# Optimization experiments

Hardware: AMD Instinct MI355X
Metric: run time of the kernel (lower is better)

## Reference

```python
import math
import jax, jax.numpy as jnp
import numpy as np

N0 = N1 = 100000
E = 200000
IN = OUT = 128
H = 8
DK = OUT // H
T = 2
R = 3


def setup_inputs() -> dict:
    key = jax.random.key(0)
    ks = jax.random.split(key, 24)
    s = 1.0 / math.sqrt(IN)
    inp = {
        'h0': jax.random.normal(ks[0], (N0, IN), jnp.float32),
        'h1': jax.random.normal(ks[1], (N1, IN), jnp.float32),
        'kw': jax.random.normal(ks[2], (T, IN, OUT), jnp.float32) * s,
        'kb': jax.random.normal(ks[3], (T, OUT), jnp.float32) * 0.01,
        'qw': jax.random.normal(ks[4], (T, IN, OUT), jnp.float32) * s,
        'qb': jax.random.normal(ks[5], (T, OUT), jnp.float32) * 0.01,
        'vw': jax.random.normal(ks[6], (T, IN, OUT), jnp.float32) * s,
        'vb': jax.random.normal(ks[7], (T, OUT), jnp.float32) * 0.01,
        'aw': jax.random.normal(ks[8], (T, OUT, OUT), jnp.float32) * (1.0 / math.sqrt(OUT)),
        'ab': jax.random.normal(ks[9], (T, OUT), jnp.float32) * 0.01,
        'rel_att': jax.random.normal(ks[10], (R, H, DK, DK), jnp.float32) * (1.0 / math.sqrt(DK)),
        'rel_msg': jax.random.normal(ks[11], (R, H, DK, DK), jnp.float32) * (1.0 / math.sqrt(DK)),
        'rel_pri': jnp.ones((R, H), jnp.float32),
        'skip': jnp.ones((T,), jnp.float32),
        'src0': jax.random.randint(ks[12], (E,), 0, N1, jnp.int32),  # author -> paper
        'dst0': jax.random.randint(ks[13], (E,), 0, N0, jnp.int32),
        'src1': jax.random.randint(ks[14], (E,), 0, N0, jnp.int32),  # paper -> author
        'dst1': jax.random.randint(ks[15], (E,), 0, N1, jnp.int32),
        'src2': jax.random.randint(ks[16], (E,), 0, N0, jnp.int32),  # paper -> paper
        'dst2': jax.random.randint(ks[17], (E,), 0, N0, jnp.int32),
    }
    return inp


def _edge_softmax(score, dst, n_dst):
    # segment softmax normalized by destination node (norm_by='dst')
    m = jax.ops.segment_max(score, dst, num_segments=n_dst)
    e = jnp.exp(score - m[dst])
    s = jax.ops.segment_sum(e, dst, num_segments=n_dst)
    return e / s[dst]


def reference(h0, h1, kw, kb, qw, qb, vw, vb, aw, ab, rel_att, rel_msg,
              rel_pri, skip, src0, dst0, src1, dst1, src2, dst2):
    n_heads, d_k = rel_att.shape[1], rel_att.shape[2]
    sqrt_dk = math.sqrt(d_k)
    hs = (h0, h1)
    Ns = (h0.shape[0], h1.shape[0])
    # per-type K/Q/V projections, reshaped to [N, H, d_k]
    k = [(hs[t] @ kw[t] + kb[t]).reshape(-1, n_heads, d_k) for t in range(2)]
    q = [(hs[t] @ qw[t] + qb[t]).reshape(-1, n_heads, d_k) for t in range(2)]
    v = [(hs[t] @ vw[t] + vb[t]).reshape(-1, n_heads, d_k) for t in range(2)]
    # (relation id, src node type, dst node type, src idx, dst idx)
    rels = ((0, 1, 0, src0, dst0), (1, 0, 1, src1, dst1), (2, 0, 0, src2, dst2))
    agg = {0: [], 1: []}
    for r, st, dt, s_idx, d_idx in rels:
        kk = jnp.einsum('nij,ijk->nik', k[st], rel_att[r])
        vv = jnp.einsum('nij,ijk->nik', v[st], rel_msg[r])
        score = (q[dt][d_idx] * kk[s_idx]).sum(-1) * rel_pri[r] / sqrt_dk  # [E,H]
        attn = _edge_softmax(score, d_idx, Ns[dt])
        msg = vv[s_idx] * attn[..., None]  # [E,H,d_k]
        agg[dt].append(jax.ops.segment_sum(msg, d_idx, num_segments=Ns[dt]))
    outs = []
    for t in range(2):
        tt = sum(agg[t]) / len(agg[t])  # cross_reducer='mean'
        tt = tt.reshape(Ns[t], n_heads * d_k)
        trans = tt @ aw[t] + ab[t]  # dropout in eval mode -> identity
        alpha = jax.nn.sigmoid(skip[t])
        outs.append(trans * alpha + hs[t] * (1.0 - alpha))
    return jnp.stack(outs)  # [2, N, out_dim] (N0 == N1)
```

## Files before the change

### kernel.cpp

```cpp
#include <hip/hip_runtime.h>
#include <stdint.h>

typedef __attribute__((ext_vector_type(8))) short s16x8;
typedef __attribute__((ext_vector_type(4))) float f32x4;

__device__ __forceinline__ ushort f2bf(float x) {
  union { float f; uint32_t u; } v; v.f = x;
  uint32_t r = v.u + 0x7FFFu + ((v.u >> 16) & 1u);
  return (ushort)(r >> 16);
}
__device__ __forceinline__ float bf2f(ushort u) {
  union { uint32_t u; float f; } v; v.u = ((uint32_t)u) << 16; return v.f;
}

__device__ __forceinline__ void barrier_lds_only() {
  asm volatile("s_waitcnt lgkmcnt(0)" ::: "memory");
  __builtin_amdgcn_s_barrier();
}

__global__ __launch_bounds__(256) void prep_weights(
    const float* __restrict__ kw, const float* __restrict__ kb,
    const float* __restrict__ qw, const float* __restrict__ qb,
    const float* __restrict__ vw, const float* __restrict__ vb,
    const float* __restrict__ aw, const float* __restrict__ ab,
    const float* __restrict__ rel_att, const float* __restrict__ rel_msg,
    ushort* __restrict__ WT, float* __restrict__ BIAS)
{
  int slot = blockIdx.x, tid = threadIdx.x;
  const float* W; const float* b; const float* rel = nullptr;
  switch (slot) {
    case 0: W = qw;         b = qb;       break;
    case 1: W = qw + 16384; b = qb + 128; break;
    case 2: W = kw + 16384; b = kb + 128; rel = rel_att + 0*2048; break;
    case 3: W = kw;         b = kb;       rel = rel_att + 1*2048; break;
    case 4: W = kw;         b = kb;       rel = rel_att + 2*2048; break;
    case 5: W = vw + 16384; b = vb + 128; rel = rel_msg + 0*2048; break;
    case 6: W = vw;         b = vb;       rel = rel_msg + 1*2048; break;
    case 7: W = vw;         b = vb;       rel = rel_msg + 2*2048; break;
    case 8: W = aw;         b = ab;       break;
    default: W = aw + 16384; b = ab + 128; break;
  }
  ushort* out = WT + slot * 16384;
  for (int e = tid; e < 16384; e += 256) {
    int c = e >> 7, k = e & 127;
    float val;
    if (!rel) {
      val = W[k*128 + c];
    } else {
      int h = c >> 4, cc = c & 15;
      float s = 0.f;
      #pragma unroll
      for (int j = 0; j < 16; j++) s += W[k*128 + h*16 + j] * rel[h*256 + j*16 + cc];
      val = s;
    }
    out[c*128 + k] = f2bf(val);
  }
  if (tid < 128) {
    int c = tid; float val;
    if (!rel) {
      val = b[c];
    } else {
      int h = c >> 4, cc = c & 15;
      float s = 0.f;
      #pragma unroll
      for (int j = 0; j < 16; j++) s += b[h*16 + j] * rel[h*256 + j*16 + cc];
      val = s;
    }
    BIAS[slot*128 + c] = val;
  }
}

__global__ __launch_bounds__(256) void proj_fused(
    const float* __restrict__ h0, const float* __restrict__ h1,
    const ushort* __restrict__ WT, const float* __restrict__ BIAS,
    ushort* __restrict__ P, int N)
{
  __shared__ ushort ALDS0[64 * 132];
  __shared__ ushort ALDS1[64 * 132];

  int src_t = blockIdx.y;
  const float* A = src_t ? h1 : h0;
  int nslots = src_t ? 3 : 5;
  unsigned smap = src_t ? 0x521u : 0x76430u;

  int tid = threadIdx.x;
  int lane = tid & 63;
  int wave = tid >> 6;
  int lr = lane & 15, lh = lane >> 4;
  int colbase = (wave & 1) * 64;
  int rowhalf = wave >> 1;

  int base = blockIdx.x * 64;
  if (base >= N) return;

  s16x8 af[2][4];
  #pragma unroll
  for (int rg = 0; rg < 2; rg++) {
    int arow = base + rowhalf*32 + rg*16 + lr;
    if (arow >= N) arow = N - 1;
    #pragma unroll
    for (int ks = 0; ks < 4; ks++) {
      const float* ap = A + (size_t)arow*128 + ks*32 + lh*8;
      f32x4 x0 = *(const f32x4*)ap;
      f32x4 x1 = *(const f32x4*)(ap + 4);
      s16x8 v;
      #pragma unroll
      for (int j = 0; j < 4; j++) { v[j] = (short)f2bf(x0[j]); v[4+j] = (short)f2bf(x1[j]); }
      af[rg][ks] = v;
    }
  }

  auto compute_slot = [&](int g, ushort* L) {
    const ushort* Bt = WT + g * 16384;
    const float* bias = BIAS + g * 128;
    #pragma unroll
    for (int ct = 0; ct < 4; ct++) {
      int col = colbase + ct*16 + lr;
      s16x8 bfr[4];
      #pragma unroll
      for (int ks = 0; ks < 4; ks++)
        bfr[ks] = *(const s16x8*)(Bt + col*128 + ks*32 + lh*8);
      float bb = bias[col];
      #pragma unroll
      for (int rg = 0; rg < 2; rg++) {
        f32x4 acc = { bb, bb, bb, bb };
        #pragma unroll
        for (int ks = 0; ks < 4; ks++)
          acc = __builtin_amdgcn_mfma_f32_16x16x32_bf16(af[rg][ks], bfr[ks], acc, 0, 0, 0);
        int rl0 = rowhalf*32 + rg*16 + lh*4;
        #pragma unroll
        for (int i = 0; i < 4; i++)
          L[(rl0 + i) * 132 + col] = f2bf(acc[i]);
      }
    }
  };

  auto copyout = [&](int g, const ushort* L) {
    ushort* C = P + (size_t)g * N * 128;
    #pragma unroll
    for (int j = 0; j < 4; j++) {
      int idx = j * 256 + tid;
      int row = idx >> 4, ch = idx & 15;
      int gr = base + row;
      if (gr < N)
        __builtin_nontemporal_store(
            *(const s16x8*)(L + row * 132 + ch * 8),
            (s16x8*)(C + (size_t)gr * 128 + ch * 8));
    }
  };

  int prev = smap & 15;
  compute_slot(prev, ALDS0);
  barrier_lds_only();
  for (int si = 1; si < nslots; si++) {
    int g = (smap >> (si * 4)) & 15;
    ushort* cur = (si & 1) ? ALDS1 : ALDS0;
    const ushort* pv = (si & 1) ? ALDS0 : ALDS1;
    copyout(prev, pv);
    compute_slot(g, cur);
    barrier_lds_only();
    prev = g;
  }
  copyout(prev, (nslots & 1) ? ALDS0 : ALDS1);
}

__global__ void count_edges(const int* __restrict__ d0, const int* __restrict__ d1,
                            const int* __restrict__ d2, int* __restrict__ counts,
                            int E, int N)
{
  int idx = blockIdx.x * 256 + threadIdx.x;
  if (idx >= 3 * E) return;
  int r = idx / E, e = idx - r * E;
  const int* D = (r == 0) ? d0 : (r == 1) ? d1 : d2;
  atomicAdd(counts + r * N + D[e], 1);
}

#define SCAN_CHUNK 2048
#define MAXC 1024

__global__ __launch_bounds__(256) void scan_partial(
    const int* __restrict__ counts, int* __restrict__ offsets,
    int* __restrict__ bsum, int N)
{
  int r = blockIdx.y, c = blockIdx.x, tid = threadIdx.x;
  const int* cnt = counts + (size_t)r * N;
  int* o = offsets + (size_t)r * (N + 1);
  int idx0 = c * SCAN_CHUNK + tid * 8;
  int p[8]; int run = 0;
  #pragma unroll
  for (int j = 0; j < 8; j++) {
    int v = (idx0 + j < N) ? cnt[idx0 + j] : 0;
    run += v; p[j] = run;
  }
  int lane = tid & 63, wid = tid >> 6;
  int x = run;
  #pragma unroll
  for (int off = 1; off < 64; off <<= 1) {
    int t = __shfl_up(x, off, 64);
    if (lane >= off) x += t;
  }
  __shared__ int wsum[4];
  if (lane == 63) wsum[wid] = x;
  __syncthreads();
  int woff = 0;
  for (int wph = 0; wph < wid; wph++) woff += wsum[wph];
  int texcl = woff + x - run;
  #pragma unroll
  for (int j = 0; j < 8; j++)
    if (idx0 + j < N) o[idx0 + j + 1] = texcl + p[j];
  if (tid == 255) bsum[r * MAXC + c] = woff + x;
}

__global__ void scan_bsums(int* __restrict__ bsum, int nchunks)
{
  int r = blockIdx.x, lane = threadIdx.x;
  int carry = 0;
  for (int base = 0; base < nchunks; base += 64) {
    int i = base + lane;
    int v0 = (i < nchunks) ? bsum[r * MAXC + i] : 0;
    int x = v0;
    #pragma unroll
    for (int off = 1; off < 64; off <<= 1) {
      int t = __shfl_up(x, off, 64);
      if (lane >= off) x += t;
    }
    if (i < nchunks) bsum[r * MAXC + i] = carry + x - v0;
    carry += __shfl(x, 63, 64);
  }
}

__global__ __launch_bounds__(256) void scan_add(
    int* __restrict__ offsets, const int* __restrict__ bsum, int N)
{
  int r = blockIdx.y, c = blockIdx.x, tid = threadIdx.x;
  int* o = offsets + (size_t)r * (N + 1);
  if (c == 0 && tid == 0) o[0] = 0;
  int add = bsum[r * MAXC + c];
  if (add == 0) return;
  int idx0 = c * SCAN_CHUNK + tid * 8;
  #pragma unroll
  for (int j = 0; j < 8; j++) {
    int i = idx0 + j;
    if (i < N) o[i + 1] += add;
  }
}

__global__ void scatter_edges(const int* __restrict__ d0, const int* __restrict__ d1,
                              const int* __restrict__ d2,
                              const int* __restrict__ offsets, int* __restrict__ cursor,
                              int* __restrict__ elist, int E, int N)
{
  int idx = blockIdx.x * 256 + threadIdx.x;
  if (idx >= 3 * E) return;
  int r = idx / E, e = idx - r * E;
  const int* D = (r == 0) ? d0 : (r == 1) ? d1 : d2;
  int dst = D[e];
  int pos = offsets[r * (N + 1) + dst] + atomicAdd(cursor + r * N + dst, 1);
  elist[r * E + pos] = e;
}

__global__ __launch_bounds__(256) void agg_final(
    const int* __restrict__ elistA, const int* __restrict__ offsA,
    const int* __restrict__ SA,
    const ushort* __restrict__ KKA, const ushort* __restrict__ VVA,
    const int* __restrict__ elistB, const int* __restrict__ offsB,
    const int* __restrict__ SB,
    const ushort* __restrict__ KKB, const ushort* __restrict__ VVB,
    int nrel, int rA, int rB,
    const ushort* __restrict__ Q, const float* __restrict__ rel_pri,
    const ushort* __restrict__ WT, const float* __restrict__ BIAS,
    const float* __restrict__ H, const float* __restrict__ skip, int t,
    float* __restrict__ outT, int N)
{
  __shared__ ushort ALDS[32 * 132];

  int tid = threadIdx.x;
  int dstl = tid >> 3, h = tid & 7;
  int dst = blockIdx.x * 32 + dstl;
  bool valid = dst < N;

  float qf[16];
  {
    const ushort* qrow = Q + (size_t)(valid ? dst : 0) * 128 + h * 16;
    s16x8 qa = *(const s16x8*)qrow;
    s16x8 qb_ = *(const s16x8*)(qrow + 8);
    #pragma unroll
    for (int j = 0; j < 8; j++) { qf[j] = bf2f((ushort)qa[j]); qf[8 + j] = bf2f((ushort)qb_[j]); }
  }

  float accT[16];
  #pragma unroll
  for (int j = 0; j < 16; j++) accT[j] = 0.f;

  {
    float pr = rel_pri[rA * 8 + h] * 0.25f;
    int b0 = valid ? offsA[dst] : 0, b1 = valid ? offsA[dst + 1] : 0;
    float sum = 0.f;
    float acc[16];
    #pragma unroll
    for (int j = 0; j < 16; j++) acc[j] = 0.f;
    for (int i = b0; i < b1; i++) {
      int e = elistA[i];
      int s = SA[e];
      const ushort* kr = KKA + (size_t)s * 128 + h * 16;
      s16x8 k0 = *(const s16x8*)kr;
      s16x8 k1 = *(const s16x8*)(kr + 8);
      float sc = 0.f;
      #pragma unroll
      for (int j = 0; j < 8; j++)
        sc += qf[j] * bf2f((ushort)k0[j]) + qf[8 + j] * bf2f((ushort)k1[j]);
      float w = __expf(sc * pr);
      const ushort* vr = VVA + (size_t)s * 128 + h * 16;
      s16x8 v0 = *(const s16x8*)vr;
      s16x8 v1 = *(const s16x8*)(vr + 8);
      #pragma unroll
      for (int j = 0; j < 8; j++) {
        acc[j]     += w * bf2f((ushort)v0[j]);
        acc[8 + j] += w * bf2f((ushort)v1[j]);
      }
      sum += w;
    }
    float inv = (b1 > b0) ? 1.0f / sum : 0.f;
    #pragma unroll
    for (int j = 0; j < 16; j++) accT[j] += acc[j] * inv;
  }
  if (nrel == 2) {
    float pr = rel_pri[rB * 8 + h] * 0.25f;
    int b0 = valid ? offsB[dst] : 0, b1 = valid ? offsB[dst + 1] : 0;
    float sum = 0.f;
    float acc[16];
    #pragma unroll
    for (int j = 0; j < 16; j++) acc[j] = 0.f;
    for (int i = b0; i < b1; i++) {
      int e = elistB[i];
      int s = SB[e];
      const ushort* kr = KKB + (size_t)s * 128 + h * 16;
      s16x8 k0 = *(const s16x8*)kr;
      s16x8 k1 = *(const s16x8*)(kr + 8);
      float sc = 0.f;
      #pragma unroll
      for (int j = 0; j < 8; j++)
        sc += qf[j] * bf2f((ushort)k0[j]) + qf[8 + j] * bf2f((ushort)k1[j]);
      float w = __expf(sc * pr);
      const ushort* vr = VVB + (size_t)s * 128 + h * 16;
      s16x8 v0 = *(const s16x8*)vr;
      s16x8 v1 = *(const s16x8*)(vr + 8);
      #pragma unroll
      for (int j = 0; j < 8; j++) {
        acc[j]     += w * bf2f((ushort)v0[j]);
        acc[8 + j] += w * bf2f((ushort)v1[j]);
      }
      sum += w;
    }
    float inv = (b1 > b0) ? 1.0f / sum : 0.f;
    #pragma unroll
    for (int j = 0; j < 16; j++) accT[j] += acc[j] * inv;
  }
  float sc = (nrel == 2) ? 0.5f : 1.0f;
  ushort* arow = ALDS + dstl * 132 + h * 16;
  #pragma unroll
  for (int j = 0; j < 16; j++) arow[j] = f2bf(accT[j] * sc);

  __syncthreads();

  int lane = tid & 63, wv = tid >> 6;
  int lr = lane & 15, lh = lane >> 4;
  int rowhalf = wv & 1, colhalf = wv >> 1;
  const ushort* Bt = WT + (8 + t) * 16384;
  const float* bias = BIAS + (8 + t) * 128;
  float alpha = 1.0f / (1.0f + __expf(-skip[t]));
  float beta = 1.0f - alpha;

  s16x8 af[4];
  int arow_l = rowhalf * 16 + lr;
  #pragma unroll
  for (int ks = 0; ks < 4; ks++)
    af[ks] = *(const s16x8*)(ALDS + arow_l * 132 + ks * 32 + lh * 8);

  #pragma unroll
  for (int ct = 0; ct < 4; ct++) {
    int col = colhalf * 64 + ct * 16 + lr;
    s16x8 bfr[4];
    #pragma unroll
    for (int ks = 0; ks < 4; ks++)
      bfr[ks] = *(const s16x8*)(Bt + col * 128 + ks * 32 + lh * 8);
    float bb = bias[col];
    f32x4 acc = { bb, bb, bb, bb };
    #pragma unroll
    for (int ks = 0; ks < 4; ks++)
      acc = __builtin_amdgcn_mfma_f32_16x16x32_bf16(af[ks], bfr[ks], acc, 0, 0, 0);
    int r0l = rowhalf * 16 + lh * 4;
    #pragma unroll
    for (int i = 0; i < 4; i++) {
      int g = blockIdx.x * 32 + r0l + i;
      if (g < N) {
        size_t off = (size_t)g * 128 + col;
        __builtin_nontemporal_store(acc[i] * alpha + H[off] * beta, &outT[off]);
      }
    }
  }
}

extern "C" void kernel_launch(void* const* d_in, const int* in_sizes, int n_in,
                              void* d_out, int out_size, void* d_ws, size_t ws_size,
                              hipStream_t stream)
{
  const float* h0      = (const float*)d_in[0];
  const float* h1      = (const float*)d_in[1];
  const float* kw      = (const float*)d_in[2];
  const float* kb      = (const float*)d_in[3];
  const float* qw      = (const float*)d_in[4];
  const float* qb      = (const float*)d_in[5];
  const float* vw      = (const float*)d_in[6];
  const float* vb      = (const float*)d_in[7];
  const float* aw      = (const float*)d_in[8];
  const float* ab      = (const float*)d_in[9];
  const float* rel_att = (const float*)d_in[10];
  const float* rel_msg = (const float*)d_in[11];
  const float* rel_pri = (const float*)d_in[12];
  const float* skip    = (const float*)d_in[13];
  const int* s0 = (const int*)d_in[14];
  const int* d0 = (const int*)d_in[15];
  const int* s1 = (const int*)d_in[16];
  const int* d1 = (const int*)d_in[17];
  const int* s2 = (const int*)d_in[18];
  const int* d2 = (const int*)d_in[19];

  int N = in_sizes[0] / 128;
  int E = in_sizes[14];

  char* w = (char*)d_ws;
  size_t o = 0;
  auto alloc = [&](size_t bytes) { size_t cur = o; o += (bytes + 255) / 256 * 256; return cur; };
  ushort* WT   = (ushort*)(w + alloc((size_t)10 * 16384 * 2));
  float*  BIAS = (float*) (w + alloc((size_t)10 * 128 * 4));
  ushort* P    = (ushort*)(w + alloc((size_t)8 * N * 128 * 2));
  int* counts  = (int*)   (w + alloc((size_t)3 * N * 4));
  int* cursor  = (int*)   (w + alloc((size_t)3 * N * 4));
  int* offs    = (int*)   (w + alloc((size_t)3 * (N + 1) * 4));
  int* elist   = (int*)   (w + alloc((size_t)3 * E * 4));
  int* bsum    = (int*)   (w + alloc((size_t)3 * MAXC * 4));
  (void)ws_size; (void)n_in; (void)out_size;

  hipMemsetAsync(counts, 0, (size_t)3 * N * 4, stream);
  hipMemsetAsync(cursor, 0, (size_t)3 * N * 4, stream);

  prep_weights<<<10, 256, 0, stream>>>(kw, kb, qw, qb, vw, vb, aw, ab,
                                       rel_att, rel_msg, WT, BIAS);

  proj_fused<<<dim3((N + 63) / 64, 2), 256, 0, stream>>>(h0, h1, WT, BIAS, P, N);

  int egrid = (3 * E + 255) / 256;
  count_edges<<<egrid, 256, 0, stream>>>(d0, d1, d2, counts, E, N);

  int nchunks = (N + SCAN_CHUNK - 1) / SCAN_CHUNK;
  scan_partial<<<dim3(nchunks, 3), 256, 0, stream>>>(counts, offs, bsum, N);
  scan_bsums<<<3, 64, 0, stream>>>(bsum, nchunks);
  scan_add<<<dim3(nchunks, 3), 256, 0, stream>>>(offs, bsum, N);

  scatter_edges<<<egrid, 256, 0, stream>>>(d0, d1, d2, offs, cursor, elist, E, N);

  int fgrid = (N + 31) / 32;
  agg_final<<<fgrid, 256, 0, stream>>>(
      elist + (size_t)0 * E, offs + (size_t)0 * (N + 1), s0,
      P + (size_t)2 * N * 128, P + (size_t)5 * N * 128,
      elist + (size_t)2 * E, offs + (size_t)2 * (N + 1), s2,
      P + (size_t)4 * N * 128, P + (size_t)7 * N * 128,
      2, 0, 2,
      P + (size_t)0 * N * 128, rel_pri,
      WT, BIAS, h0, skip, 0, (float*)d_out, N);
  agg_final<<<fgrid, 256, 0, stream>>>(
      elist + (size_t)1 * E, offs + (size_t)1 * (N + 1), s1,
      P + (size_t)3 * N * 128, P + (size_t)6 * N * 128,
      elist + (size_t)1 * E, offs + (size_t)1 * (N + 1), s1,
      P + (size_t)3 * N * 128, P + (size_t)6 * N * 128,
      1, 1, 1,
      P + (size_t)1 * N * 128, rel_pri,
      WT, BIAS, h1, skip, 1, (float*)d_out + (size_t)N * 128, N);
}
```

Baseline: 414.5 us.

## Fold relation matrices into query and output weights instead of per-source K/V

Moves the per-relation att matrix from the key side onto the query (q·W_att^T) and the per-relation msg matrix into the output projection (W_msg·aw), so only plain K and V per node type are projected and stored (4 slabs instead of 8). The per-relation query projections are computed inside the aggregation kernel with MFMA from H rows, and the final projection sums two relation-specific GEMMs. This halves the projection GEMM work and projected-feature traffic, at the cost of extra MFMA work and LDS buffers in the aggregation kernel.

```diff
diff --git a/kernel.cpp b/kernel.cpp
--- a/kernel.cpp
+++ b/kernel.cpp
@@ -27,44 +27,50 @@
     ushort* __restrict__ WT, float* __restrict__ BIAS)
 {
   int slot = blockIdx.x, tid = threadIdx.x;
-  const float* W; const float* b; const float* rel = nullptr;
+  const float* W; const float* b; const float* rel = nullptr; int mode;
   switch (slot) {
-    case 0: W = qw;         b = qb;       break;
-    case 1: W = qw + 16384; b = qb + 128; break;
-    case 2: W = kw + 16384; b = kb + 128; rel = rel_att + 0*2048; break;
-    case 3: W = kw;         b = kb;       rel = rel_att + 1*2048; break;
-    case 4: W = kw;         b = kb;       rel = rel_att + 2*2048; break;
-    case 5: W = vw + 16384; b = vb + 128; rel = rel_msg + 0*2048; break;
-    case 6: W = vw;         b = vb;       rel = rel_msg + 1*2048; break;
-    case 7: W = vw;         b = vb;       rel = rel_msg + 2*2048; break;
-    case 8: W = aw;         b = ab;       break;
-    default: W = aw + 16384; b = ab + 128; break;
+    case 0: W = kw;         b = kb;       mode = 0; break;
+    case 1: W = kw + 16384; b = kb + 128; mode = 0; break;
+    case 2: W = vw;         b = vb;       mode = 0; break;
+    case 3: W = vw + 16384; b = vb + 128; mode = 0; break;
+    case 4: W = qw;         b = qb;       rel = rel_att;        mode = 1; break;
+    case 5: W = qw + 16384; b = qb + 128; rel = rel_att + 2048; mode = 1; break;
+    case 6: W = qw;         b = qb;       rel = rel_att + 4096; mode = 1; break;
+    case 7: W = aw;         b = ab;       rel = rel_msg;        mode = 2; break;
+    case 8: W = aw + 16384; b = ab + 128; rel = rel_msg + 2048; mode = 2; break;
+    default: W = aw;        b = ab;       rel = rel_msg + 4096; mode = 2; break;
   }
   ushort* out = WT + slot * 16384;
   for (int e = tid; e < 16384; e += 256) {
     int c = e >> 7, k = e & 127;
     float val;
-    if (!rel) {
+    if (mode == 0) {
       val = W[k*128 + c];
-    } else {
+    } else if (mode == 1) {
       int h = c >> 4, cc = c & 15;
       float s = 0.f;
       #pragma unroll
-      for (int j = 0; j < 16; j++) s += W[k*128 + h*16 + j] * rel[h*256 + j*16 + cc];
+      for (int j = 0; j < 16; j++) s += W[k*128 + h*16 + j] * rel[h*256 + cc*16 + j];
+      val = s;
+    } else {
+      int hr = k >> 4, ir = k & 15;
+      float s = 0.f;
+      #pragma unroll
+      for (int j = 0; j < 16; j++) s += rel[hr*256 + ir*16 + j] * W[(hr*16 + j)*128 + c];
       val = s;
     }
     out[c*128 + k] = f2bf(val);
   }
   if (tid < 128) {
     int c = tid; float val;
-    if (!rel) {
-      val = b[c];
-    } else {
+    if (mode == 1) {
       int h = c >> 4, cc = c & 15;
       float s = 0.f;
       #pragma unroll
-      for (int j = 0; j < 16; j++) s += b[h*16 + j] * rel[h*256 + j*16 + cc];
+      for (int j = 0; j < 16; j++) s += b[h*16 + j] * rel[h*256 + cc*16 + j];
       val = s;
+    } else {
+      val = b[c];
     }
     BIAS[slot*128 + c] = val;
   }
@@ -80,8 +86,8 @@
 
   int src_t = blockIdx.y;
   const float* A = src_t ? h1 : h0;
-  int nslots = src_t ? 3 : 5;
-  unsigned smap = src_t ? 0x521u : 0x76430u;
+  unsigned smap = src_t ? 0x31u : 0x20u;
+  const int nslots = 2;
 
   int tid = threadIdx.x;
   int lane = tid & 63;
@@ -154,14 +160,12 @@
   barrier_lds_only();
   for (int si = 1; si < nslots; si++) {
     int g = (smap >> (si * 4)) & 15;
-    ushort* cur = (si & 1) ? ALDS1 : ALDS0;
-    const ushort* pv = (si & 1) ? ALDS0 : ALDS1;
-    copyout(prev, pv);
-    compute_slot(g, cur);
+    copyout(prev, ALDS0);
+    compute_slot(g, ALDS1);
     barrier_lds_only();
     prev = g;
   }
-  copyout(prev, (nslots & 1) ? ALDS0 : ALDS1);
+  copyout(prev, ALDS1);
 }
 
 __global__ void count_edges(const int* __restrict__ d0, const int* __restrict__ d1,
@@ -262,140 +266,222 @@
 __global__ __launch_bounds__(256) void agg_final(
     const int* __restrict__ elistA, const int* __restrict__ offsA,
     const int* __restrict__ SA,
-    const ushort* __restrict__ KKA, const ushort* __restrict__ VVA,
+    const ushort* __restrict__ KA, const ushort* __restrict__ VA,
     const int* __restrict__ elistB, const int* __restrict__ offsB,
     const int* __restrict__ SB,
-    const ushort* __restrict__ KKB, const ushort* __restrict__ VVB,
+    const ushort* __restrict__ KB, const ushort* __restrict__ VB,
     int nrel, int rA, int rB,
-    const ushort* __restrict__ Q, const float* __restrict__ rel_pri,
+    int qslotA, int qslotB, int fslotA, int fslotB,
     const ushort* __restrict__ WT, const float* __restrict__ BIAS,
-    const float* __restrict__ H, const float* __restrict__ skip, int t,
+    const float* __restrict__ H, const float* __restrict__ rel_pri,
+    const float* __restrict__ skip, int t,
     float* __restrict__ outT, int N)
 {
-  __shared__ ushort ALDS[32 * 132];
+  __shared__ ushort T0[32 * 132];
+  __shared__ ushort T1[32 * 132];
 
   int tid = threadIdx.x;
+  int lane = tid & 63, wv = tid >> 6;
+  int lr = lane & 15, lh = lane >> 4;
+  int rowhalf = wv & 1, colhalf = wv >> 1;
+  int base = blockIdx.x * 32;
+
+  s16x8 af[4];
+  {
+    int arow = base + rowhalf*16 + lr;
+    if (arow >= N) arow = N - 1;
+    #pragma unroll
+    for (int ks = 0; ks < 4; ks++) {
+      const float* ap = H + (size_t)arow*128 + ks*32 + lh*8;
+      f32x4 x0 = *(const f32x4*)ap;
+      f32x4 x1 = *(const f32x4*)(ap + 4);
+      s16x8 v;
+      #pragma unroll
+      for (int j = 0; j < 4; j++) { v[j] = (short)f2bf(x0[j]); v[4+j] = (short)f2bf(x1[j]); }
+      af[ks] = v;
+    }
+  }
+  {
+    const ushort* Bt = WT + qslotA * 16384;
+    const float* bq = BIAS + qslotA * 128;
+    #pragma unroll
+    for (int ct = 0; ct < 4; ct++) {
+      int col = colhalf*64 + ct*16 + lr;
+      s16x8 bfr[4];
+      #pragma unroll
+      for (int ks = 0; ks < 4; ks++)
+        bfr[ks] = *(const s16x8*)(Bt + col*128 + ks*32 + lh*8);
+      float bb = bq[col];
+      f32x4 acc = { bb, bb, bb, bb };
+      #pragma unroll
+      for (int ks = 0; ks < 4; ks++)
+        acc = __builtin_amdgcn_mfma_f32_16x16x32_bf16(af[ks], bfr[ks], acc, 0, 0, 0);
+      int r0l = rowhalf*16 + lh*4;
+      #pragma unroll
+      for (int i = 0; i < 4; i++) T0[(r0l + i)*132 + col] = f2bf(acc[i]);
+    }
+  }
+  if (nrel == 2) {
+    const ushort* Bt = WT + qslotB * 16384;
+    const float* bq = BIAS + qslotB * 128;
+    #pragma unroll
+    for (int ct = 0; ct < 4; ct++) {
+      int col = colhalf*64 + ct*16 + lr;
+      s16x8 bfr[4];
+      #pragma unroll
+      for (int ks = 0; ks < 4; ks++)
+        bfr[ks] = *(const s16x8*)(Bt + col*128 + ks*32 + lh*8);
+      float bb = bq[col];
+      f32x4 acc = { bb, bb, bb, bb };
+      #pragma unroll
+      for (int ks = 0; ks < 4; ks++)
+        acc = __builtin_amdgcn_mfma_f32_16x16x32_bf16(af[ks], bfr[ks], acc, 0, 0, 0);
+      int r0l = rowhalf*16 + lh*4;
+      #pragma unroll
+      for (int i = 0; i < 4; i++) T1[(r0l + i)*132 + col] = f2bf(acc[i]);
+    }
+  }
+  __syncthreads();
+
   int dstl = tid >> 3, h = tid & 7;
-  int dst = blockIdx.x * 32 + dstl;
+  int dst = base + dstl;
   bool valid = dst < N;
 
-  float qf[16];
+  float qfA[16], qfB[16];
   {
-    const ushort* qrow = Q + (size_t)(valid ? dst : 0) * 128 + h * 16;
-    s16x8 qa = *(const s16x8*)qrow;
-    s16x8 qb_ = *(const s16x8*)(qrow + 8);
-    #pragma unroll
-    for (int j = 0; j < 8; j++) { qf[j] = bf2f((ushort)qa[j]); qf[8 + j] = bf2f((ushort)qb_[j]); }
-  }
-
-  float accT[16];
-  #pragma unroll
-  for (int j = 0; j < 16; j++) accT[j] = 0.f;
-
+    const ushort* qr = T0 + dstl*132 + h*16;
+    #pragma unroll
+    for (int j = 0; j < 16; j++) qfA[j] = bf2f(qr[j]);
+  }
+  if (nrel == 2) {
+    const ushort* qr = T1 + dstl*132 + h*16;
+    #pragma unroll
+    for (int j = 0; j < 16; j++) qfB[j] = bf2f(qr[j]);
+  }
+  __syncthreads();
+
+  float accA[16], accB[16];
   {
-    float pr = rel_pri[rA * 8 + h] * 0.25f;
+    float pr = rel_pri[rA*8 + h] * 0.25f;
     int b0 = valid ? offsA[dst] : 0, b1 = valid ? offsA[dst + 1] : 0;
     float sum = 0.f;
-    float acc[16];
-    #pragma unroll
-    for (int j = 0; j < 16; j++) acc[j] = 0.f;
+    #pragma unroll
+    for (int j = 0; j < 16; j++) accA[j] = 0.f;
     for (int i = b0; i < b1; i++) {
       int e = elistA[i];
       int s = SA[e];
-      const ushort* kr = KKA + (size_t)s * 128 + h * 16;
+      const ushort* kr = KA + (size_t)s*128 + h*16;
       s16x8 k0 = *(const s16x8*)kr;
       s16x8 k1 = *(const s16x8*)(kr + 8);
       float sc = 0.f;
       #pragma unroll
       for (int j = 0; j < 8; j++)
-        sc += qf[j] * bf2f((ushort)k0[j]) + qf[8 + j] * bf2f((ushort)k1[j]);
+        sc += qfA[j]*bf2f((ushort)k0[j]) + qfA[8+j]*bf2f((ushort)k1[j]);
       float w = __expf(sc * pr);
-      const ushort* vr = VVA + (size_t)s * 128 + h * 16;
+      const ushort* vr = VA + (size_t)s*128 + h*16;
       s16x8 v0 = *(const s16x8*)vr;
       s16x8 v1 = *(const s16x8*)(vr + 8);
       #pragma unroll
       for (int j = 0; j < 8; j++) {
-        acc[j]     += w * bf2f((ushort)v0[j]);
-        acc[8 + j] += w * bf2f((ushort)v1[j]);
+        accA[j]   += w * bf2f((ushort)v0[j]);
+        accA[8+j] += w * bf2f((ushort)v1[j]);
       }
       sum += w;
     }
     float inv = (b1 > b0) ? 1.0f / sum : 0.f;
     #pragma unroll
-    for (int j = 0; j < 16; j++) accT[j] += acc[j] * inv;
+    for (int j = 0; j < 16; j++) accA[j] *= inv;
   }
   if (nrel == 2) {
-    float pr = rel_pri[rB * 8 + h] * 0.25f;
+    float pr = rel_pri[rB*8 + h] * 0.25f;
     int b0 = valid ? offsB[dst] : 0, b1 = valid ? offsB[dst + 1] : 0;
     float sum = 0.f;
-    float acc[16];
-    #pragma unroll
-    for (int j = 0; j < 16; j++) acc[j] = 0.f;
+    #pragma unroll
+    for (int j = 0; j < 16; j++) accB[j] = 0.f;
     for (int i = b0; i < b1; i++) {
       int e = elistB[i];
       int s = SB[e];
-      const ushort* kr = KKB + (size_t)s * 128 + h * 16;
+      const ushort* kr = KB + (size_t)s*128 + h*16;
       s16x8 k0 = *(const s16x8*)kr;
       s16x8 k1 = *(const s16x8*)(kr + 8);
       float sc = 0.f;
       #pragma unroll
       for (int j = 0; j < 8; j++)
-        sc += qf[j] * bf2f((ushort)k0[j]) + qf[8 + j] * bf2f((ushort)k1[j]);
+        sc += qfB[j]*bf2f((ushort)k0[j]) + qfB[8+j]*bf2f((ushort)k1[j]);
       float w = __expf(sc * pr);
-      const ushort* vr = VVB + (size_t)s * 128 + h * 16;
+      const ushort* vr = VB + (size_t)s*128 + h*16;
       s16x8 v0 = *(const s16x8*)vr;
       s16x8 v1 = *(const s16x8*)(vr + 8);
       #pragma unroll
       for (int j = 0; j < 8; j++) {
-        acc[j]     += w * bf2f((ushort)v0[j]);
-        acc[8 + j] += w * bf2f((ushort)v1[j]);
+        accB[j]   += w * bf2f((ushort)v0[j]);
+        accB[8+j] += w * bf2f((ushort)v1[j]);
       }
       sum += w;
     }
     float inv = (b1 > b0) ? 1.0f / sum : 0.f;
     #pragma unroll
-    for (int j = 0; j < 16; j++) accT[j] += acc[j] * inv;
-  }
-  float sc = (nrel == 2) ? 0.5f : 1.0f;
-  ushort* arow = ALDS + dstl * 132 + h * 16;
-  #pragma unroll
-  for (int j = 0; j < 16; j++) arow[j] = f2bf(accT[j] * sc);
-
+    for (int j = 0; j < 16; j++) accB[j] *= inv;
+  }
+  {
+    ushort* a0 = T0 + dstl*132 + h*16;
+    #pragma unroll
+    for (int j = 0; j < 16; j++) a0[j] = f2bf(accA[j]);
+    if (nrel == 2) {
+      ushort* a1 = T1 + dstl*132 + h*16;
+      #pragma unroll
+      for (int j = 0; j < 16; j++) a1[j] = f2bf(accB[j]);
+    }
+  }
   __syncthreads();
 
-  int lane = tid & 63, wv = tid >> 6;
-  int lr = lane & 15, lh = lane >> 4;
-  int rowhalf = wv & 1, colhalf = wv >> 1;
-  const ushort* Bt = WT + (8 + t) * 16384;
-  const float* bias = BIAS + (8 + t) * 128;
+  const float* bias = BIAS + fslotA * 128;
   float alpha = 1.0f / (1.0f + __expf(-skip[t]));
   float beta = 1.0f - alpha;
-
-  s16x8 af[4];
-  int arow_l = rowhalf * 16 + lr;
+  float rscale = (nrel == 2) ? 0.5f : 1.0f;
+
+  s16x8 afA[4], afB[4];
+  int arow_l = rowhalf*16 + lr;
   #pragma unroll
   for (int ks = 0; ks < 4; ks++)
-    af[ks] = *(const s16x8*)(ALDS + arow_l * 132 + ks * 32 + lh * 8);
+    afA[ks] = *(const s16x8*)(T0 + arow_l*132 + ks*32 + lh*8);
+  if (nrel == 2) {
+    #pragma unroll
+    for (int ks = 0; ks < 4; ks++)
+      afB[ks] = *(const s16x8*)(T1 + arow_l*132 + ks*32 + lh*8);
+  }
 
   #pragma unroll
   for (int ct = 0; ct < 4; ct++) {
-    int col = colhalf * 64 + ct * 16 + lr;
-    s16x8 bfr[4];
+    int col = colhalf*64 + ct*16 + lr;
+    s16x8 bfrA[4];
+    const ushort* BtA = WT + fslotA * 16384;
     #pragma unroll
     for (int ks = 0; ks < 4; ks++)
-      bfr[ks] = *(const s16x8*)(Bt + col * 128 + ks * 32 + lh * 8);
+      bfrA[ks] = *(const s16x8*)(BtA + col*128 + ks*32 + lh*8);
+    f32x4 acc = { 0.f, 0.f, 0.f, 0.f };
+    #pragma unroll
+    for (int ks = 0; ks < 4; ks++)
+      acc = __builtin_amdgcn_mfma_f32_16x16x32_bf16(afA[ks], bfrA[ks], acc, 0, 0, 0);
+    if (nrel == 2) {
+      const ushort* BtB = WT + fslotB * 16384;
+      s16x8 bfrB[4];
+      #pragma unroll
+      for (int ks = 0; ks < 4; ks++)
+        bfrB[ks] = *(const s16x8*)(BtB + col*128 + ks*32 + lh*8);
+      #pragma unroll
+      for (int ks = 0; ks < 4; ks++)
+        acc = __builtin_amdgcn_mfma_f32_16x16x32_bf16(afB[ks], bfrB[ks], acc, 0, 0, 0);
+    }
     float bb = bias[col];
-    f32x4 acc = { bb, bb, bb, bb };
-    #pragma unroll
-    for (int ks = 0; ks < 4; ks++)
-      acc = __builtin_amdgcn_mfma_f32_16x16x32_bf16(af[ks], bfr[ks], acc, 0, 0, 0);
-    int r0l = rowhalf * 16 + lh * 4;
+    int r0l = rowhalf*16 + lh*4;
     #pragma unroll
     for (int i = 0; i < 4; i++) {
-      int g = blockIdx.x * 32 + r0l + i;
+      int g = base + r0l + i;
       if (g < N) {
-        size_t off = (size_t)g * 128 + col;
-        __builtin_nontemporal_store(acc[i] * alpha + H[off] * beta, &outT[off]);
+        size_t off = (size_t)g*128 + col;
+        __builtin_nontemporal_store((acc[i]*rscale + bb)*alpha + H[off]*beta,
+                                    &outT[off]);
       }
     }
   }
@@ -434,7 +520,7 @@
   auto alloc = [&](size_t bytes) { size_t cur = o; o += (bytes + 255) / 256 * 256; return cur; };
   ushort* WT   = (ushort*)(w + alloc((size_t)10 * 16384 * 2));
   float*  BIAS = (float*) (w + alloc((size_t)10 * 128 * 4));
-  ushort* P    = (ushort*)(w + alloc((size_t)8 * N * 128 * 2));
+  ushort* P    = (ushort*)(w + alloc((size_t)4 * N * 128 * 2));
   int* counts  = (int*)   (w + alloc((size_t)3 * N * 4));
   int* cursor  = (int*)   (w + alloc((size_t)3 * N * 4));
   int* offs    = (int*)   (w + alloc((size_t)3 * (N + 1) * 4));
@@ -461,20 +547,18 @@
   scatter_edges<<<egrid, 256, 0, stream>>>(d0, d1, d2, offs, cursor, elist, E, N);
 
   int fgrid = (N + 31) / 32;
+  const ushort* K0 = P + (size_t)0 * N * 128;
+  const ushort* K1 = P + (size_t)1 * N * 128;
+  const ushort* V0 = P + (size_t)2 * N * 128;
+  const ushort* V1 = P + (size_t)3 * N * 128;
   agg_final<<<fgrid, 256, 0, stream>>>(
-      elist + (size_t)0 * E, offs + (size_t)0 * (N + 1), s0,
-      P + (size_t)2 * N * 128, P + (size_t)5 * N * 128,
-      elist + (size_t)2 * E, offs + (size_t)2 * (N + 1), s2,
-      P + (size_t)4 * N * 128, P + (size_t)7 * N * 128,
-      2, 0, 2,
-      P + (size_t)0 * N * 128, rel_pri,
-      WT, BIAS, h0, skip, 0, (float*)d_out, N);
+      elist + (size_t)0 * E, offs + (size_t)0 * (N + 1), s0, K1, V1,
+      elist + (size_t)2 * E, offs + (size_t)2 * (N + 1), s2, K0, V0,
+      2, 0, 2, 4, 6, 7, 9,
+      WT, BIAS, h0, rel_pri, skip, 0, (float*)d_out, N);
   agg_final<<<fgrid, 256, 0, stream>>>(
-      elist + (size_t)1 * E, offs + (size_t)1 * (N + 1), s1,
-      P + (size_t)3 * N * 128, P + (size_t)6 * N * 128,
-      elist + (size_t)1 * E, offs + (size_t)1 * (N + 1), s1,
-      P + (size_t)3 * N * 128, P + (size_t)6 * N * 128,
-      1, 1, 1,
-      P + (size_t)1 * N * 128, rel_pri,
-      WT, BIAS, h1, skip, 1, (float*)d_out + (size_t)N * 128, N);
-}
+      elist + (size_t)1 * E, offs + (size_t)1 * (N + 1), s1, K0, V0,
+      elist + (size_t)1 * E, offs + (size_t)1 * (N + 1), s1, K0, V0,
+      1, 1, 1, 5, 5, 8, 8,
+      WT, BIAS, h1, rel_pri, skip, 1, (float*)d_out + (size_t)N * 128, N);
+}
```

Measured after the change: 442.5 us. 6.8% more time.

## Fold relation matrices into Q and output weights, store source ids in CSR

Applied to the files above, without the earlier changes.

The relation attention matrix is now folded into the Q projection and the relation message matrix into the output projection, so K and V are computed once per node type. This drops one projection (8 to 7 slabs) and lets the two relations sharing paper sources read the same K/V. The edge list now stores source ids directly, removing an indirection per edge. The gather loop prefetches the next edge's K/V rows, and both node types run in one 2D launch. For type 0 the output GEMM is done as two MFMA passes, one per relation. The trade-off is extra per-block GEMM work and more register pressure.

```diff
diff --git a/kernel.cpp b/kernel.cpp
--- a/kernel.cpp
+++ b/kernel.cpp
@@ -27,44 +27,50 @@
     ushort* __restrict__ WT, float* __restrict__ BIAS)
 {
   int slot = blockIdx.x, tid = threadIdx.x;
-  const float* W; const float* b; const float* rel = nullptr;
+  const float* W; const float* b; const float* rel = nullptr; int mode;
   switch (slot) {
-    case 0: W = qw;         b = qb;       break;
-    case 1: W = qw + 16384; b = qb + 128; break;
-    case 2: W = kw + 16384; b = kb + 128; rel = rel_att + 0*2048; break;
-    case 3: W = kw;         b = kb;       rel = rel_att + 1*2048; break;
-    case 4: W = kw;         b = kb;       rel = rel_att + 2*2048; break;
-    case 5: W = vw + 16384; b = vb + 128; rel = rel_msg + 0*2048; break;
-    case 6: W = vw;         b = vb;       rel = rel_msg + 1*2048; break;
-    case 7: W = vw;         b = vb;       rel = rel_msg + 2*2048; break;
-    case 8: W = aw;         b = ab;       break;
-    default: W = aw + 16384; b = ab + 128; break;
+    case 0: W = kw;         b = kb;       mode = 0; break;
+    case 1: W = kw + 16384; b = kb + 128; mode = 0; break;
+    case 2: W = vw;         b = vb;       mode = 0; break;
+    case 3: W = vw + 16384; b = vb + 128; mode = 0; break;
+    case 4: W = qw;         b = qb;       rel = rel_att;        mode = 1; break;
+    case 5: W = qw + 16384; b = qb + 128; rel = rel_att + 2048; mode = 1; break;
+    case 6: W = qw;         b = qb;       rel = rel_att + 4096; mode = 1; break;
+    case 7: W = aw;         b = ab;       rel = rel_msg;        mode = 2; break;
+    case 8: W = aw + 16384; b = ab + 128; rel = rel_msg + 2048; mode = 2; break;
+    default: W = aw;        b = ab;       rel = rel_msg + 4096; mode = 2; break;
   }
   ushort* out = WT + slot * 16384;
   for (int e = tid; e < 16384; e += 256) {
     int c = e >> 7, k = e & 127;
     float val;
-    if (!rel) {
+    if (mode == 0) {
       val = W[k*128 + c];
-    } else {
+    } else if (mode == 1) {
       int h = c >> 4, cc = c & 15;
       float s = 0.f;
       #pragma unroll
-      for (int j = 0; j < 16; j++) s += W[k*128 + h*16 + j] * rel[h*256 + j*16 + cc];
+      for (int j = 0; j < 16; j++) s += W[k*128 + h*16 + j] * rel[h*256 + cc*16 + j];
+      val = s;
+    } else {
+      int hr = k >> 4, ir = k & 15;
+      float s = 0.f;
+      #pragma unroll
+      for (int j = 0; j < 16; j++) s += rel[hr*256 + ir*16 + j] * W[(hr*16 + j)*128 + c];
       val = s;
     }
     out[c*128 + k] = f2bf(val);
   }
   if (tid < 128) {
     int c = tid; float val;
-    if (!rel) {
-      val = b[c];
-    } else {
+    if (mode == 1) {
       int h = c >> 4, cc = c & 15;
       float s = 0.f;
       #pragma unroll
-      for (int j = 0; j < 16; j++) s += b[h*16 + j] * rel[h*256 + j*16 + cc];
+      for (int j = 0; j < 16; j++) s += b[h*16 + j] * rel[h*256 + cc*16 + j];
       val = s;
+    } else {
+      val = b[c];
     }
     BIAS[slot*128 + c] = val;
   }
@@ -80,8 +86,8 @@
 
   int src_t = blockIdx.y;
   const float* A = src_t ? h1 : h0;
-  int nslots = src_t ? 3 : 5;
-  unsigned smap = src_t ? 0x521u : 0x76430u;
+  int nslots = src_t ? 3 : 4;
+  unsigned smap = src_t ? 0x531u : 0x6420u;
 
   int tid = threadIdx.x;
   int lane = tid & 63;
@@ -247,155 +253,199 @@
 
 __global__ void scatter_edges(const int* __restrict__ d0, const int* __restrict__ d1,
                               const int* __restrict__ d2,
+                              const int* __restrict__ s0, const int* __restrict__ s1,
+                              const int* __restrict__ s2,
                               const int* __restrict__ offsets, int* __restrict__ cursor,
-                              int* __restrict__ elist, int E, int N)
+                              int* __restrict__ slist, int E, int N)
 {
   int idx = blockIdx.x * 256 + threadIdx.x;
   if (idx >= 3 * E) return;
   int r = idx / E, e = idx - r * E;
   const int* D = (r == 0) ? d0 : (r == 1) ? d1 : d2;
+  const int* S = (r == 0) ? s0 : (r == 1) ? s1 : s2;
   int dst = D[e];
   int pos = offsets[r * (N + 1) + dst] + atomicAdd(cursor + r * N + dst, 1);
-  elist[r * E + pos] = e;
+  slist[r * E + pos] = S[e];
 }
 
 __global__ __launch_bounds__(256) void agg_final(
-    const int* __restrict__ elistA, const int* __restrict__ offsA,
-    const int* __restrict__ SA,
-    const ushort* __restrict__ KKA, const ushort* __restrict__ VVA,
-    const int* __restrict__ elistB, const int* __restrict__ offsB,
-    const int* __restrict__ SB,
-    const ushort* __restrict__ KKB, const ushort* __restrict__ VVB,
-    int nrel, int rA, int rB,
-    const ushort* __restrict__ Q, const float* __restrict__ rel_pri,
+    const int* __restrict__ slist, const int* __restrict__ offs,
+    const ushort* __restrict__ P,
     const ushort* __restrict__ WT, const float* __restrict__ BIAS,
-    const float* __restrict__ H, const float* __restrict__ skip, int t,
-    float* __restrict__ outT, int N)
-{
-  __shared__ ushort ALDS[32 * 132];
-
+    const float* __restrict__ h0, const float* __restrict__ h1,
+    const float* __restrict__ rel_pri, const float* __restrict__ skip,
+    float* __restrict__ out, int N, int E)
+{
+  __shared__ ushort T0[32 * 132];
+  __shared__ ushort T1[32 * 132];
+
+  int ty = blockIdx.y;
   int tid = threadIdx.x;
   int dstl = tid >> 3, h = tid & 7;
-  int dst = blockIdx.x * 32 + dstl;
+  int base = blockIdx.x * 32;
+  int dst = base + dstl;
   bool valid = dst < N;
-
-  float qf[16];
+  const float* H = ty ? h1 : h0;
+  float* outT = out + (size_t)ty * N * 128;
+
+  const ushort* K0 = P;
+  const ushort* K1 = P + (size_t)1 * N * 128;
+  const ushort* V0 = P + (size_t)2 * N * 128;
+  const ushort* V1 = P + (size_t)3 * N * 128;
+
   {
-    const ushort* qrow = Q + (size_t)(valid ? dst : 0) * 128 + h * 16;
-    s16x8 qa = *(const s16x8*)qrow;
-    s16x8 qb_ = *(const s16x8*)(qrow + 8);
-    #pragma unroll
-    for (int j = 0; j < 8; j++) { qf[j] = bf2f((ushort)qa[j]); qf[8 + j] = bf2f((ushort)qb_[j]); }
-  }
-
-  float accT[16];
-  #pragma unroll
-  for (int j = 0; j < 16; j++) accT[j] = 0.f;
-
-  {
+    int rA = ty ? 1 : 0;
+    const int* sl = slist + (size_t)rA * E;
+    const int* of = offs + (size_t)rA * (N + 1);
+    const ushort* K = ty ? K0 : K1;
+    const ushort* V = ty ? V0 : V1;
+    const ushort* QT = P + (size_t)(ty ? 5 : 4) * N * 128;
+
+    float qf[16];
+    const ushort* qr = QT + (size_t)(valid ? dst : 0) * 128 + h * 16;
+    #pragma unroll
+    for (int j = 0; j < 16; j++) qf[j] = bf2f(qr[j]);
     float pr = rel_pri[rA * 8 + h] * 0.25f;
-    int b0 = valid ? offsA[dst] : 0, b1 = valid ? offsA[dst + 1] : 0;
+
+    float acc[16];
+    #pragma unroll
+    for (int j = 0; j < 16; j++) acc[j] = 0.f;
     float sum = 0.f;
+    int b0 = valid ? of[dst] : 0, b1 = valid ? of[dst + 1] : 0;
+    if (b1 > b0) {
+      int scur = sl[b0];
+      const ushort* kr = K + (size_t)scur * 128 + h * 16;
+      const ushort* vr = V + (size_t)scur * 128 + h * 16;
+      s16x8 k0 = *(const s16x8*)kr, k1 = *(const s16x8*)(kr + 8);
+      s16x8 v0 = *(const s16x8*)vr, v1 = *(const s16x8*)(vr + 8);
+      for (int i = b0; i < b1; i++) {
+        int snx = (i + 1 < b1) ? sl[i + 1] : scur;
+        const ushort* krn = K + (size_t)snx * 128 + h * 16;
+        const ushort* vrn = V + (size_t)snx * 128 + h * 16;
+        s16x8 k0n = *(const s16x8*)krn, k1n = *(const s16x8*)(krn + 8);
+        s16x8 v0n = *(const s16x8*)vrn, v1n = *(const s16x8*)(vrn + 8);
+        float sc = 0.f;
+        #pragma unroll
+        for (int j = 0; j < 8; j++)
+          sc += qf[j] * bf2f((ushort)k0[j]) + qf[8+j] * bf2f((ushort)k1[j]);
+        float w = __expf(sc * pr);
+        #pragma unroll
+        for (int j = 0; j < 8; j++) {
+          acc[j]   += w * bf2f((ushort)v0[j]);
+          acc[8+j] += w * bf2f((ushort)v1[j]);
+        }
+        sum += w;
+        k0 = k0n; k1 = k1n; v0 = v0n; v1 = v1n;
+      }
+    }
+    float inv = (b1 > b0) ? 1.0f / sum : 0.f;
+    ushort* a0 = T0 + dstl * 132 + h * 16;
+    #pragma unroll
+    for (int j = 0; j < 16; j++) a0[j] = f2bf(acc[j] * inv);
+  }
+
+  if (ty == 0) {
+    const int* sl = slist + (size_t)2 * E;
+    const int* of = offs + (size_t)2 * (N + 1);
+    const ushort* K = K0;
+    const ushort* V = V0;
+    const ushort* QT = P + (size_t)6 * N * 128;
+
+    float qf[16];
+    const ushort* qr = QT + (size_t)(valid ? dst : 0) * 128 + h * 16;
+    #pragma unroll
+    for (int j = 0; j < 16; j++) qf[j] = bf2f(qr[j]);
+    float pr = rel_pri[2 * 8 + h] * 0.25f;
+
     float acc[16];
     #pragma unroll
     for (int j = 0; j < 16; j++) acc[j] = 0.f;
-    for (int i = b0; i < b1; i++) {
-      int e = elistA[i];
-      int s = SA[e];
-      const ushort* kr = KKA + (size_t)s * 128 + h * 16;
-      s16x8 k0 = *(const s16x8*)kr;
-      s16x8 k1 = *(const s16x8*)(kr + 8);
-      float sc = 0.f;
-      #pragma unroll
-      for (int j = 0; j < 8; j++)
-        sc += qf[j] * bf2f((ushort)k0[j]) + qf[8 + j] * bf2f((ushort)k1[j]);
-      float w = __expf(sc * pr);
-      const ushort* vr = VVA + (size_t)s * 128 + h * 16;
-      s16x8 v0 = *(const s16x8*)vr;
-      s16x8 v1 = *(const s16x8*)(vr + 8);
-      #pragma unroll
-      for (int j = 0; j < 8; j++) {
-        acc[j]     += w * bf2f((ushort)v0[j]);
-        acc[8 + j] += w * bf2f((ushort)v1[j]);
+    float sum = 0.f;
+    int b0 = valid ? of[dst] : 0, b1 = valid ? of[dst + 1] : 0;
+    if (b1 > b0) {
+      int scur = sl[b0];
+      const ushort* kr = K + (size_t)scur * 128 + h * 16;
+      const ushort* vr = V + (size_t)scur * 128 + h * 16;
+      s16x8 k0 = *(const s16x8*)kr, k1 = *(const s16x8*)(kr + 8);
+      s16x8 v0 = *(const s16x8*)vr, v1 = *(const s16x8*)(vr + 8);
+      for (int i = b0; i < b1; i++) {
+        int snx = (i + 1 < b1) ? sl[i + 1] : scur;
+        const ushort* krn = K + (size_t)snx * 128 + h * 16;
+        const ushort* vrn = V + (size_t)snx * 128 + h * 16;
+        s16x8 k0n = *(const s16x8*)krn, k1n = *(const s16x8*)(krn + 8);
+        s16x8 v0n = *(const s16x8*)vrn, v1n = *(const s16x8*)(vrn + 8);
+        float sc = 0.f;
+        #pragma unroll
+        for (int j = 0; j < 8; j++)
+          sc += qf[j] * bf2f((ushort)k0[j]) + qf[8+j] * bf2f((ushort)k1[j]);
+        float w = __expf(sc * pr);
+        #pragma unroll
+        for (int j = 0; j < 8; j++) {
+          acc[j]   += w * bf2f((ushort)v0[j]);
+          acc[8+j] += w * bf2f((ushort)v1[j]);
+        }
+        sum += w;
+        k0 = k0n; k1 = k1n; v0 = v0n; v1 = v1n;
       }
-      sum += w;
     }
     float inv = (b1 > b0) ? 1.0f / sum : 0.f;
-    #pragma unroll
-    for (int j = 0; j < 16; j++) accT[j] += acc[j] * inv;
-  }
-  if (nrel == 2) {
-    float pr = rel_pri[rB * 8 + h] * 0.25f;
-    int b0 = valid ? offsB[dst] : 0, b1 = valid ? offsB[dst + 1] : 0;
-    float sum = 0.f;
-    float acc[16];
-    #pragma unroll
-    for (int j = 0; j < 16; j++) acc[j] = 0.f;
-    for (int i = b0; i < b1; i++) {
-      int e = elistB[i];
-      int s = SB[e];
-      const ushort* kr = KKB + (size_t)s * 128 + h * 16;
-      s16x8 k0 = *(const s16x8*)kr;
-      s16x8 k1 = *(const s16x8*)(kr + 8);
-      float sc = 0.f;
-      #pragma unroll
-      for (int j = 0; j < 8; j++)
-        sc += qf[j] * bf2f((ushort)k0[j]) + qf[8 + j] * bf2f((ushort)k1[j]);
-      float w = __expf(sc * pr);
-      const ushort* vr = VVB + (size_t)s * 128 + h * 16;
-      s16x8 v0 = *(const s16x8*)vr;
-      s16x8 v1 = *(const s16x8*)(vr + 8);
-      #pragma unroll
-      for (int j = 0; j < 8; j++) {
-        acc[j]     += w * bf2f((ushort)v0[j]);
-        acc[8 + j] += w * bf2f((ushort)v1[j]);
-      }
-      sum += w;
-    }
-    float inv = (b1 > b0) ? 1.0f / sum : 0.f;
-    #pragma unroll
-    for (int j = 0; j < 16; j++) accT[j] += acc[j] * inv;
-  }
-  float sc = (nrel == 2) ? 0.5f : 1.0f;
-  ushort* arow = ALDS + dstl * 132 + h * 16;
-  #pragma unroll
-  for (int j = 0; j < 16; j++) arow[j] = f2bf(accT[j] * sc);
-
+    ushort* a1 = T1 + dstl * 132 + h * 16;
+    #pragma unroll
+    for (int j = 0; j < 16; j++) a1[j] = f2bf(acc[j] * inv);
+  }
   __syncthreads();
 
   int lane = tid & 63, wv = tid >> 6;
   int lr = lane & 15, lh = lane >> 4;
   int rowhalf = wv & 1, colhalf = wv >> 1;
-  const ushort* Bt = WT + (8 + t) * 16384;
-  const float* bias = BIAS + (8 + t) * 128;
-  float alpha = 1.0f / (1.0f + __expf(-skip[t]));
+  int fA = ty ? 8 : 7;
+  const float* bias = BIAS + fA * 128;
+  float alpha = 1.0f / (1.0f + __expf(-skip[ty]));
   float beta = 1.0f - alpha;
-
-  s16x8 af[4];
+  float rscale = ty ? 1.0f : 0.5f;
+
+  s16x8 afA[4], afB[4];
   int arow_l = rowhalf * 16 + lr;
   #pragma unroll
   for (int ks = 0; ks < 4; ks++)
-    af[ks] = *(const s16x8*)(ALDS + arow_l * 132 + ks * 32 + lh * 8);
+    afA[ks] = *(const s16x8*)(T0 + arow_l * 132 + ks * 32 + lh * 8);
+  if (ty == 0) {
+    #pragma unroll
+    for (int ks = 0; ks < 4; ks++)
+      afB[ks] = *(const s16x8*)(T1 + arow_l * 132 + ks * 32 + lh * 8);
+  }
 
   #pragma unroll
   for (int ct = 0; ct < 4; ct++) {
     int col = colhalf * 64 + ct * 16 + lr;
-    s16x8 bfr[4];
+    const ushort* BtA = WT + fA * 16384;
+    s16x8 bfrA[4];
     #pragma unroll
     for (int ks = 0; ks < 4; ks++)
-      bfr[ks] = *(const s16x8*)(Bt + col * 128 + ks * 32 + lh * 8);
+      bfrA[ks] = *(const s16x8*)(BtA + col * 128 + ks * 32 + lh * 8);
+    f32x4 acc = { 0.f, 0.f, 0.f, 0.f };
+    #pragma unroll
+    for (int ks = 0; ks < 4; ks++)
+      acc = __builtin_amdgcn_mfma_f32_16x16x32_bf16(afA[ks], bfrA[ks], acc, 0, 0, 0);
+    if (ty == 0) {
+      const ushort* BtB = WT + 9 * 16384;
+      s16x8 bfrB[4];
+      #pragma unroll
+      for (int ks = 0; ks < 4; ks++)
+        bfrB[ks] = *(const s16x8*)(BtB + col * 128 + ks * 32 + lh * 8);
+      #pragma unroll
+      for (int ks = 0; ks < 4; ks++)
+        acc = __builtin_amdgcn_mfma_f32_16x16x32_bf16(afB[ks], bfrB[ks], acc, 0, 0, 0);
+    }
     float bb = bias[col];
-    f32x4 acc = { bb, bb, bb, bb };
-    #pragma unroll
-    for (int ks = 0; ks < 4; ks++)
-      acc = __builtin_amdgcn_mfma_f32_16x16x32_bf16(af[ks], bfr[ks], acc, 0, 0, 0);
     int r0l = rowhalf * 16 + lh * 4;
     #pragma unroll
     for (int i = 0; i < 4; i++) {
-      int g = blockIdx.x * 32 + r0l + i;
+      int g = base + r0l + i;
       if (g < N) {
         size_t off = (size_t)g * 128 + col;
-        __builtin_nontemporal_store(acc[i] * alpha + H[off] * beta, &outT[off]);
+        __builtin_nontemporal_store((acc[i] * rscale + bb) * alpha + H[off] * beta,
+                                    &outT[off]);
       }
     }
   }
@@ -434,11 +484,11 @@
   auto alloc = [&](size_t bytes) { size_t cur = o; o += (bytes + 255) / 256 * 256; return cur; };
   ushort* WT   = (ushort*)(w + alloc((size_t)10 * 16384 * 2));
   float*  BIAS = (float*) (w + alloc((size_t)10 * 128 * 4));
-  ushort* P    = (ushort*)(w + alloc((size_t)8 * N * 128 * 2));
+  ushort* P    = (ushort*)(w + alloc((size_t)7 * N * 128 * 2));
   int* counts  = (int*)   (w + alloc((size_t)3 * N * 4));
   int* cursor  = (int*)   (w + alloc((size_t)3 * N * 4));
   int* offs    = (int*)   (w + alloc((size_t)3 * (N + 1) * 4));
-  int* elist   = (int*)   (w + alloc((size_t)3 * E * 4));
+  int* slist   = (int*)   (w + alloc((size_t)3 * E * 4));
   int* bsum    = (int*)   (w + alloc((size_t)3 * MAXC * 4));
   (void)ws_size; (void)n_in; (void)out_size;
 
@@ -458,23 +508,11 @@
   scan_bsums<<<3, 64, 0, stream>>>(bsum, nchunks);
   scan_add<<<dim3(nchunks, 3), 256, 0, stream>>>(offs, bsum, N);
 
-  scatter_edges<<<egrid, 256, 0, stream>>>(d0, d1, d2, offs, cursor, elist, E, N);
+  scatter_edges<<<egrid, 256, 0, stream>>>(d0, d1, d2, s0, s1, s2,
+                                           offs, cursor, slist, E, N);
 
   int fgrid = (N + 31) / 32;
-  agg_final<<<fgrid, 256, 0, stream>>>(
-      elist + (size_t)0 * E, offs + (size_t)0 * (N + 1), s0,
-      P + (size_t)2 * N * 128, P + (size_t)5 * N * 128,
-      elist + (size_t)2 * E, offs + (size_t)2 * (N + 1), s2,
-      P + (size_t)4 * N * 128, P + (size_t)7 * N * 128,
-      2, 0, 2,
-      P + (size_t)0 * N * 128, rel_pri,
-      WT, BIAS, h0, skip, 0, (float*)d_out, N);
-  agg_final<<<fgrid, 256, 0, stream>>>(
-      elist + (size_t)1 * E, offs + (size_t)1 * (N + 1), s1,
-      P + (size_t)3 * N * 128, P + (size_t)6 * N * 128,
-      elist + (size_t)1 * E, offs + (size_t)1 * (N + 1), s1,
-      P + (size_t)3 * N * 128, P + (size_t)6 * N * 128,
-      1, 1, 1,
-      P + (size_t)1 * N * 128, rel_pri,
-      WT, BIAS, h1, skip, 1, (float*)d_out + (size_t)N * 128, N);
-}
+  agg_final<<<dim3(fgrid, 2), 256, 0, stream>>>(
+      slist, offs, P, WT, BIAS, h0, h1, rel_pri, skip,
+      (float*)d_out, N, E);
+}
```

Result: faster. 360.1 us (-13.1%).
